# Optimization experiments

Measured on AMD Instinct MI355X. Metric: run time of the kernel, lower is better.

## Reference

```python
import jax, jax.numpy as jnp
import numpy as np

N = 100000   # nodes
D = 64       # node_emb_dim
R = 8        # num relations
E = 1600000  # edges (avg degree 16)


def setup_inputs() -> dict:
    key = jax.random.key(0)
    k1, k2, k3, k4, k5 = jax.random.split(key, 5)
    x = jax.random.normal(k1, (N, D), dtype=jnp.float32)
    edge_index = jax.random.randint(k2, (2, E), 0, N, dtype=jnp.int64)
    edge_type = jax.random.randint(k3, (E,), 0, R, dtype=jnp.int64)
    W_rel = jax.random.normal(k4, (R, D, D), dtype=jnp.float32) / np.sqrt(D)
    W_root = jax.random.normal(k5, (D, D), dtype=jnp.float32) / np.sqrt(D)
    bias = jnp.zeros((D,), dtype=jnp.float32)
    return {"x": x, "edge_index": edge_index, "edge_type": edge_type,
            "W_rel": W_rel, "W_root": W_root, "bias": bias}


def reference(x, edge_index, edge_type, W_rel, W_root, bias):
    # PyG RGCNConv: per-relation linear transform of source nodes,
    # mean-aggregated per (target node, relation), plus root transform + bias.
    n_nodes, d = x.shape
    n_rel = W_rel.shape[0]
    src, dst = edge_index[0], edge_index[1]

    # Transform every node under every relation once: [N, R, D]
    h_all = jnp.einsum('nd,rde->nre', x, W_rel)
    # Gather per-edge message: [E, D]
    msg = h_all[src, edge_type]

    # Per-(dst, relation) in-degree counts for mean normalization
    cnt = jnp.zeros((n_nodes, n_rel), dtype=x.dtype).at[dst, edge_type].add(1.0)
    norm = 1.0 / jnp.maximum(cnt[dst, edge_type], 1.0)  # [E]

    # Scatter-add normalized messages to target nodes
    agg = jnp.zeros((n_nodes, d), dtype=x.dtype).at[dst].add(msg * norm[:, None])

    out = agg + x @ W_root + bias
    return (out, edge_index, edge_type)
```

## Files before the change

### kernel.cpp

```cpp
#include <hip/hip_runtime.h>

#define DD 64
#define RR 8
#define KA 576
#define NT 18
#define NPART 8
#define ECH 2048
#define TILE 32

typedef short bf16x8 __attribute__((ext_vector_type(8)));
typedef float f32x4  __attribute__((ext_vector_type(4)));

__device__ __forceinline__ float bf2f(unsigned short u) {
    union { unsigned u; float f; } c; c.u = ((unsigned)u) << 16; return c.f;
}
__device__ __forceinline__ unsigned short f2bf(float f) {
    union { float f; unsigned u; } c; c.f = f;
    unsigned u = c.u;
    u += 0x7FFF + ((u >> 16) & 1);
    return (unsigned short)(u >> 16);
}

__global__ void k_xcast(const float* __restrict__ x, unsigned short* __restrict__ xb,
                        int N)
{
    int i = blockIdx.x * 256 + threadIdx.x;
    int total = (N + 1) * (DD / 4);
    if (i >= total) return;
    ushort4 o;
    if (i < N * (DD / 4)) {
        float4 f = ((const float4*)x)[i];
        o = make_ushort4(f2bf(f.x), f2bf(f.y), f2bf(f.z), f2bf(f.w));
    } else {
        o = make_ushort4(0, 0, 0, 0);
    }
    ((ushort4*)xb)[i] = o;
}

__global__ __launch_bounds__(256) void k_count_rank(
    const int* __restrict__ ei, const int* __restrict__ et,
    int* __restrict__ cnt, unsigned* __restrict__ rr, int E)
{
    const int base = blockIdx.x * ECH + threadIdx.x;
    int d[8], t[8], rk[8]; bool m[8];
    #pragma unroll
    for (int j = 0; j < 8; ++j) {
        int e = base + j * 256;
        m[j] = (e < E);
        d[j] = m[j] ? ei[E + e] : 0;
    }
    #pragma unroll
    for (int j = 0; j < 8; ++j) {
        int e = base + j * 256;
        if (m[j]) t[j] = et[e];
    }
    #pragma unroll
    for (int j = 0; j < 8; ++j)
        if (m[j]) rk[j] = atomicAdd(&cnt[(size_t)d[j] * RR + t[j]], 1);
    #pragma unroll
    for (int j = 0; j < 8; ++j) {
        int e = base + j * 256;
        if (m[j]) rr[e] = (unsigned)rk[j] | ((unsigned)t[j] << 24);
    }
}

__global__ __launch_bounds__(256) void k_alloc(
    const int* __restrict__ cnt, int* __restrict__ startv,
    int* __restrict__ start2, int* __restrict__ counter,
    int* __restrict__ sorted, int N)
{
    __shared__ int sdata[256];
    __shared__ int sbase;
    const int tid = threadIdx.x;
    const int n = blockIdx.x * 256 + tid;

    int deg = 0, deg8 = 0;
    int c[RR];
    if (n < N) {
        const int4* c4 = (const int4*)(cnt + (size_t)n * RR);
        int4 a = c4[0], b = c4[1];
        c[0]=a.x; c[1]=a.y; c[2]=a.z; c[3]=a.w;
        c[4]=b.x; c[5]=b.y; c[6]=b.z; c[7]=b.w;
        #pragma unroll
        for (int r = 0; r < RR; ++r) deg += c[r];
        deg8 = (deg + 7) & ~7;
    }
    sdata[tid] = deg8;
    __syncthreads();
    int v = deg8;
    #pragma unroll
    for (int off = 1; off < 256; off <<= 1) {
        int t = (tid >= off) ? sdata[tid - off] : 0;
        __syncthreads();
        v += t;
        sdata[tid] = v;
        __syncthreads();
    }
    if (tid == 255) sbase = atomicAdd(counter, v);
    __syncthreads();
    if (n < N) {
        int st = sbase + v - deg8;
        startv[n] = st;
        int h = st;
        #pragma unroll
        for (int r = 0; r < RR; ++r) { start2[(size_t)n * RR + r] = h; h += c[r]; }
        for (int j = deg; j < deg8; ++j) sorted[st + j] = N;
    }
}

__global__ __launch_bounds__(256) void k_scatter_part(
    const int* __restrict__ ei, const unsigned* __restrict__ rr,
    const int* __restrict__ start2, int* __restrict__ sorted, int E, int N)
{
    const int p    = blockIdx.x & (NPART - 1);
    const int sb   = blockIdx.x / NPART;
    const int dlo  = (int)((long long)N * p / NPART);
    const int dhi  = (int)((long long)N * (p + 1) / NPART);
    const int base = sb * ECH + threadIdx.x;

    int d[8]; bool m[8]; unsigned q[8]; int s[8], st[8];
    #pragma unroll
    for (int j = 0; j < 8; ++j) {
        int e = base + j * 256;
        d[j] = (e < E) ? ei[E + e] : -1;
    }
    #pragma unroll
    for (int j = 0; j < 8; ++j) m[j] = (d[j] >= dlo && d[j] < dhi);
    #pragma unroll
    for (int j = 0; j < 8; ++j) {
        int e = base + j * 256;
        if (m[j]) { q[j] = rr[e]; s[j] = ei[e]; }
    }
    #pragma unroll
    for (int j = 0; j < 8; ++j)
        if (m[j]) st[j] = start2[(size_t)d[j] * RR + (q[j] >> 24)];
    #pragma unroll
    for (int j = 0; j < 8; ++j)
        if (m[j]) sorted[st[j] + (q[j] & 0xFFFFFFu)] = s[j];
}

__global__ void k_packW(const float* __restrict__ Wrel, const float* __restrict__ Wroot,
                        unsigned short* __restrict__ Bh)
{
    int idx = blockIdx.x * 256 + threadIdx.x;
    if (idx >= NT * 4 * 64 * 8) return;
    int i    = idx & 7;
    int lane = (idx >> 3) & 63;
    int f    = (idx >> 9) & 3;
    int t    = idx >> 11;
    int k = t * 32 + (lane >> 4) * 8 + i;
    int d = f * 16 + (lane & 15);
    int r = k >> 6, kk = k & 63;
    float w = (r < RR) ? Wrel[((size_t)r * DD + kk) * DD + d]
                       : Wroot[(size_t)kk * DD + d];
    Bh[idx] = f2bf(w);
}

__global__ __launch_bounds__(512) void k_agg_mfma(
    const unsigned short* __restrict__ xb, const int* __restrict__ sorted,
    const int* __restrict__ startv, const int* __restrict__ cnt,
    const unsigned short* __restrict__ Bh, const float* __restrict__ bias,
    float* __restrict__ out, int N)
{
    __shared__ __align__(16) unsigned short As[TILE * KA];
    const int nb   = blockIdx.x * TILE;
    const int wv   = threadIdx.x >> 6;
    const int lane = threadIdx.x & 63;

    for (int i = 0; i < 4; ++i) {
        const int row = wv * 4 + i;
        const int dst = nb + row;
        if (dst >= N) break;

        const int xsh = (row & 7) << 3;
        unsigned short* ao = As + row * KA;

        const int cv = cnt[(size_t)dst * RR + (lane & 7)];
        int deg = 0;
        #pragma unroll
        for (int r = 0; r < RR; ++r) deg += __builtin_amdgcn_readlane(cv, r);
        const int deg8 = (deg + 7) & ~7;

        const int s0  = __builtin_amdgcn_readfirstlane(startv[dst]);
        const int end = s0 + deg8;

        int   r      = 0;
        int   c_r    = __builtin_amdgcn_readlane(cv, 0);
        int   next_b = s0 + c_r;
        float cur    = 0.f;

        auto flush = [&]() {
            float inv = __builtin_amdgcn_rcpf(fmaxf((float)c_r, 1.f));
            ao[(r * DD + lane) ^ xsh] = f2bf(cur * inv);
            cur = 0.f;
            ++r;
            c_r = __builtin_amdgcn_readlane(cv, r & 7);
            next_b += c_r;
        };

        int e = s0;
        int wbase = s0;
        int vidx  = sorted[wbase + lane];
        while (e < end) {
            if (e - wbase >= 64) {
                wbase = e;
                vidx  = sorted[wbase + lane];
            }
            const int k    = e - wbase;
            const int take = min(end - e, 64 - k);
            for (int ii = 0; ii < take; ii += 8) {
                int q0 = __builtin_amdgcn_readlane(vidx, k + ii + 0);
                int q1 = __builtin_amdgcn_readlane(vidx, k + ii + 1);
                int q2 = __builtin_amdgcn_readlane(vidx, k + ii + 2);
                int q3 = __builtin_amdgcn_readlane(vidx, k + ii + 3);
                int q4 = __builtin_amdgcn_readlane(vidx, k + ii + 4);
                int q5 = __builtin_amdgcn_readlane(vidx, k + ii + 5);
                int q6 = __builtin_amdgcn_readlane(vidx, k + ii + 6);
                int q7 = __builtin_amdgcn_readlane(vidx, k + ii + 7);
                unsigned short u0 = xb[(size_t)q0 * DD + lane];
                unsigned short u1 = xb[(size_t)q1 * DD + lane];
                unsigned short u2 = xb[(size_t)q2 * DD + lane];
                unsigned short u3 = xb[(size_t)q3 * DD + lane];
                unsigned short u4 = xb[(size_t)q4 * DD + lane];
                unsigned short u5 = xb[(size_t)q5 * DD + lane];
                unsigned short u6 = xb[(size_t)q6 * DD + lane];
                unsigned short u7 = xb[(size_t)q7 * DD + lane];
                const int base = e + ii;
                while (base + 0 == next_b && r < RR) flush();
                cur += bf2f(u0);
                while (base + 1 == next_b && r < RR) flush();
                cur += bf2f(u1);
                while (base + 2 == next_b && r < RR) flush();
                cur += bf2f(u2);
                while (base + 3 == next_b && r < RR) flush();
                cur += bf2f(u3);
                while (base + 4 == next_b && r < RR) flush();
                cur += bf2f(u4);
                while (base + 5 == next_b && r < RR) flush();
                cur += bf2f(u5);
                while (base + 6 == next_b && r < RR) flush();
                cur += bf2f(u6);
                while (base + 7 == next_b && r < RR) flush();
                cur += bf2f(u7);
            }
            e += take;
        }
        while (r < RR) flush();

        ao[(8 * DD + lane) ^ xsh] = xb[(size_t)dst * DD + lane];
    }

    __syncthreads();

    const int rlo = lane & 15;
    const int kg  = lane >> 4;
    const int rg  = (wv & 1) * 16;
    const int cf  = wv >> 1;
    const int row = rg + rlo;
    const int xsh = (row & 7) << 3;

    f32x4 acc = {0.f,0.f,0.f,0.f};

    const unsigned short* arow = As + row * KA;
    #pragma unroll
    for (int t = 0; t < NT; ++t) {
        bf16x8 a = *(const bf16x8*)(arow + ((t * 32 + kg * 8) ^ xsh));
        bf16x8 b = *(const bf16x8*)(Bh + (size_t)t * 2048 + (size_t)cf * 512
                                       + lane * 8);
        acc = __builtin_amdgcn_mfma_f32_16x16x32_bf16(a, b, acc, 0, 0, 0);
    }

    const float bl = bias[rlo + cf * 16];
    const int orow = nb + rg + kg * 4;
    #pragma unroll
    for (int j = 0; j < 4; ++j) {
        int rr2 = orow + j;
        if (rr2 < N) out[(size_t)rr2 * DD + rlo + cf * 16] = acc[j] + bl;
    }
}

__global__ void k_echo(const int* __restrict__ ei, const int* __restrict__ et,
                       float* __restrict__ out_ei, float* __restrict__ out_et,
                       int E)
{
    int i = blockIdx.x * 256 + threadIdx.x;
    if (i < 2 * E) out_ei[i] = (float)ei[i];
    if (i < E)     out_et[i] = (float)et[i];
}

extern "C" void kernel_launch(void* const* d_in, const int* in_sizes, int n_in,
                              void* d_out, int out_size, void* d_ws, size_t ws_size,
                              hipStream_t stream)
{
    const float* x     = (const float*)d_in[0];
    const int*   ei    = (const int*)d_in[1];
    const int*   et    = (const int*)d_in[2];
    const float* Wrel  = (const float*)d_in[3];
    const float* Wroot = (const float*)d_in[4];
    const float* bias  = (const float*)d_in[5];

    const int N = in_sizes[0] / DD;
    const int E = in_sizes[2];
    const int M = N * RR;

    float* out    = (float*)d_out;
    float* out_ei = out + (size_t)N * DD;
    float* out_et = out_ei + (size_t)2 * E;

    auto align = [](size_t v) { return (v + 255) & ~(size_t)255; };

    size_t p = 0;
    int* cnt = (int*)((char*)d_ws + p);              p += align((size_t)M * 4);
    int* counter = (int*)((char*)d_ws + p);
    size_t zero_bytes = p + 256;                     p += 256;
    int* startv = (int*)((char*)d_ws + p);           p += align((size_t)N * 4);
    int* start2 = (int*)((char*)d_ws + p);           p += align((size_t)M * 4);
    unsigned* rr = (unsigned*)((char*)d_ws + p);     p += align((size_t)E * 4);
    int* sorted = (int*)((char*)d_ws + p);           p += align(((size_t)E + 7*(size_t)N + 128) * 4);
    unsigned short* xb = (unsigned short*)((char*)d_ws + p); p += align(((size_t)N + 1) * DD * 2);
    unsigned short* Bh = (unsigned short*)((char*)d_ws + p); p += align((size_t)NT*4*64*8*2);

    hipMemsetAsync(d_ws, 0, zero_bytes, stream);

    const int nsb = (E + ECH - 1) / ECH;

    k_xcast <<<dim3(((N + 1) * (DD/4) + 255) / 256), 256, 0, stream>>>(x, xb, N);
    k_packW <<<dim3((NT*4*64*8 + 255) / 256), 256, 0, stream>>>(Wrel, Wroot, Bh);
    k_count_rank <<<dim3(nsb), 256, 0, stream>>>(ei, et, cnt, rr, E);
    k_alloc <<<dim3((N + 255) / 256), 256, 0, stream>>>(cnt, startv, start2,
                                                        counter, sorted, N);
    k_scatter_part<<<dim3(nsb * NPART), 256, 0, stream>>>(ei, rr, start2, sorted, E, N);

    k_agg_mfma<<<dim3((N + TILE - 1) / TILE), 512, 0, stream>>>(
        xb, sorted, startv, cnt, Bh, bias, out, N);

    k_echo<<<dim3((2 * E + 255) / 256), 256, 0, stream>>>(ei, et, out_ei, out_et, E);
}
```

Measured before the change: 224.2 us.

## Fuse edge echo into count kernel and gather four nodes per wave in one stream

The separate echo kernel is removed. Its float conversion of edge_index and edge_type is folded into the count/rank kernel, which already loads dst and type, so only src needs an extra read. The aggregation now treats each wave's four consecutive destination nodes as one contiguous segment of 32 relation runs, relying on those nodes being laid out contiguously with their padding in sorted order. This removes a kernel launch and repeated index loads, and lets the gather pipeline cross node boundaries. The cost is more complex boundary and padding bookkeeping in the flush logic.

```diff
diff --git a/kernel.cpp b/kernel.cpp
--- a/kernel.cpp
+++ b/kernel.cpp
@@ -37,12 +37,13 @@
     ((ushort4*)xb)[i] = o;
 }
 
-__global__ __launch_bounds__(256) void k_count_rank(
+__global__ __launch_bounds__(256) void k_count_rank_echo(
     const int* __restrict__ ei, const int* __restrict__ et,
-    int* __restrict__ cnt, unsigned* __restrict__ rr, int E)
+    int* __restrict__ cnt, unsigned* __restrict__ rr,
+    float* __restrict__ out_ei, float* __restrict__ out_et, int E)
 {
     const int base = blockIdx.x * ECH + threadIdx.x;
-    int d[8], t[8], rk[8]; bool m[8];
+    int d[8], t[8], s[8], rk[8]; bool m[8];
     #pragma unroll
     for (int j = 0; j < 8; ++j) {
         int e = base + j * 256;
@@ -52,7 +53,7 @@
     #pragma unroll
     for (int j = 0; j < 8; ++j) {
         int e = base + j * 256;
-        if (m[j]) t[j] = et[e];
+        if (m[j]) { t[j] = et[e]; s[j] = ei[e]; }
     }
     #pragma unroll
     for (int j = 0; j < 8; ++j)
@@ -60,7 +61,12 @@
     #pragma unroll
     for (int j = 0; j < 8; ++j) {
         int e = base + j * 256;
-        if (m[j]) rr[e] = (unsigned)rk[j] | ((unsigned)t[j] << 24);
+        if (m[j]) {
+            rr[e] = (unsigned)rk[j] | ((unsigned)t[j] << 24);
+            out_ei[e]     = (float)s[j];
+            out_ei[E + e] = (float)d[j];
+            out_et[e]     = (float)t[j];
+        }
     }
 }
 
@@ -167,35 +173,45 @@
     const int wv   = threadIdx.x >> 6;
     const int lane = threadIdx.x & 63;
 
-    for (int i = 0; i < 4; ++i) {
-        const int row = wv * 4 + i;
-        const int dst = nb + row;
-        if (dst >= N) break;
-
-        const int xsh = (row & 7) << 3;
-        unsigned short* ao = As + row * KA;
-
-        const int cv = cnt[(size_t)dst * RR + (lane & 7)];
-        int deg = 0;
+    const int row0 = wv * 4;
+    const int dst0 = nb + row0;
+    const int nv   = min(4, N - dst0);
+    if (nv > 0) {
+        int cidx = lane & 31;
+        if (cidx >= nv * 8) cidx = nv * 8 - 1;
+        const int cv = cnt[(size_t)dst0 * RR + cidx];
+
+        int pads = 0, total = 0;
         #pragma unroll
-        for (int r = 0; r < RR; ++r) deg += __builtin_amdgcn_readlane(cv, r);
-        const int deg8 = (deg + 7) & ~7;
-
-        const int s0  = __builtin_amdgcn_readfirstlane(startv[dst]);
-        const int end = s0 + deg8;
-
-        int   r      = 0;
-        int   c_r    = __builtin_amdgcn_readlane(cv, 0);
-        int   next_b = s0 + c_r;
+        for (int i = 0; i < 4; ++i) {
+            if (i < nv) {
+                int deg = 0;
+                #pragma unroll
+                for (int r = 0; r < RR; ++r)
+                    deg += __builtin_amdgcn_readlane(cv, i * 8 + r);
+                int d8 = (deg + 7) & ~7;
+                pads  |= (d8 - deg) << (3 * i);
+                total += d8;
+            }
+        }
+        const int nrun = nv * 8;
+        const int s0   = __builtin_amdgcn_readfirstlane(startv[dst0]);
+        const int end  = s0 + total;
+
+        int   rl     = 0;
+        int   next_b = s0 + __builtin_amdgcn_readlane(cv, 0);
         float cur    = 0.f;
 
         auto flush = [&]() {
-            float inv = __builtin_amdgcn_rcpf(fmaxf((float)c_r, 1.f));
-            ao[(r * DD + lane) ^ xsh] = f2bf(cur * inv);
+            const int c = __builtin_amdgcn_readlane(cv, rl & 31);
+            const float inv = __builtin_amdgcn_rcpf(fmaxf((float)c, 1.f));
+            const int row = row0 + (rl >> 3);
+            As[row * KA + (((rl & 7) * DD + lane) ^ ((row & 7) << 3))]
+                = f2bf(cur * inv);
             cur = 0.f;
-            ++r;
-            c_r = __builtin_amdgcn_readlane(cv, r & 7);
-            next_b += c_r;
+            ++rl;
+            const int cn = __builtin_amdgcn_readlane(cv, rl & 31);
+            next_b += cn + (((rl & 7) == 7) ? ((pads >> (3 * (rl >> 3))) & 7) : 0);
         };
 
         int e = s0;
@@ -226,28 +242,35 @@
                 unsigned short u6 = xb[(size_t)q6 * DD + lane];
                 unsigned short u7 = xb[(size_t)q7 * DD + lane];
                 const int base = e + ii;
-                while (base + 0 == next_b && r < RR) flush();
+                while (base + 0 == next_b && rl < nrun) flush();
                 cur += bf2f(u0);
-                while (base + 1 == next_b && r < RR) flush();
+                while (base + 1 == next_b && rl < nrun) flush();
                 cur += bf2f(u1);
-                while (base + 2 == next_b && r < RR) flush();
+                while (base + 2 == next_b && rl < nrun) flush();
                 cur += bf2f(u2);
-                while (base + 3 == next_b && r < RR) flush();
+                while (base + 3 == next_b && rl < nrun) flush();
                 cur += bf2f(u3);
-                while (base + 4 == next_b && r < RR) flush();
+                while (base + 4 == next_b && rl < nrun) flush();
                 cur += bf2f(u4);
-                while (base + 5 == next_b && r < RR) flush();
+                while (base + 5 == next_b && rl < nrun) flush();
                 cur += bf2f(u5);
-                while (base + 6 == next_b && r < RR) flush();
+                while (base + 6 == next_b && rl < nrun) flush();
                 cur += bf2f(u6);
-                while (base + 7 == next_b && r < RR) flush();
+                while (base + 7 == next_b && rl < nrun) flush();
                 cur += bf2f(u7);
             }
             e += take;
         }
-        while (r < RR) flush();
-
-        ao[(8 * DD + lane) ^ xsh] = xb[(size_t)dst * DD + lane];
+        while (rl < nrun) flush();
+
+        #pragma unroll
+        for (int i = 0; i < 4; ++i) {
+            if (i < nv) {
+                const int row = row0 + i;
+                As[row * KA + ((8 * DD + lane) ^ ((row & 7) << 3))]
+                    = xb[(size_t)(dst0 + i) * DD + lane];
+            }
+        }
     }
 
     __syncthreads();
@@ -277,15 +300,6 @@
         int rr2 = orow + j;
         if (rr2 < N) out[(size_t)rr2 * DD + rlo + cf * 16] = acc[j] + bl;
     }
-}
-
-__global__ void k_echo(const int* __restrict__ ei, const int* __restrict__ et,
-                       float* __restrict__ out_ei, float* __restrict__ out_et,
-                       int E)
-{
-    int i = blockIdx.x * 256 + threadIdx.x;
-    if (i < 2 * E) out_ei[i] = (float)ei[i];
-    if (i < E)     out_et[i] = (float)et[i];
 }
 
 extern "C" void kernel_launch(void* const* d_in, const int* in_sizes, int n_in,
@@ -326,13 +340,12 @@
 
     k_xcast <<<dim3(((N + 1) * (DD/4) + 255) / 256), 256, 0, stream>>>(x, xb, N);
     k_packW <<<dim3((NT*4*64*8 + 255) / 256), 256, 0, stream>>>(Wrel, Wroot, Bh);
-    k_count_rank <<<dim3(nsb), 256, 0, stream>>>(ei, et, cnt, rr, E);
+    k_count_rank_echo <<<dim3(nsb), 256, 0, stream>>>(ei, et, cnt, rr,
+                                                      out_ei, out_et, E);
     k_alloc <<<dim3((N + 255) / 256), 256, 0, stream>>>(cnt, startv, start2,
                                                         counter, sorted, N);
     k_scatter_part<<<dim3(nsb * NPART), 256, 0, stream>>>(ei, rr, start2, sorted, E, N);
 
     k_agg_mfma<<<dim3((N + TILE - 1) / TILE), 512, 0, stream>>>(
         xb, sorted, startv, cnt, Bh, bias, out, N);
-
-    k_echo<<<dim3((2 * E + 255) / 256), 256, 0, stream>>>(ei, et, out_ei, out_et, E);
-}
+}
```

After: 234.3 us. 1.05x slower.

## Fuse edge echo into count kernel and batch per-wave count/start loads

Applied to the files above, without the earlier changes.

The separate echo kernel that converts edge_index and edge_type to float is removed. That conversion now happens inside the count/rank kernel, which already reads dst and type and now also reads src. This saves one launch and a second full read of the edge arrays. In the aggregation kernel, each wave now loads the counts and start offsets for its four rows with one vector load and extracts them with readlane, instead of issuing per-row loads. The trade-off is extra register pressure and more stores in the count kernel, which is atomic-bound.

```diff
diff --git a/kernel.cpp b/kernel.cpp
--- a/kernel.cpp
+++ b/kernel.cpp
@@ -37,12 +37,13 @@
     ((ushort4*)xb)[i] = o;
 }
 
-__global__ __launch_bounds__(256) void k_count_rank(
+__global__ __launch_bounds__(256) void k_count_rank_echo(
     const int* __restrict__ ei, const int* __restrict__ et,
-    int* __restrict__ cnt, unsigned* __restrict__ rr, int E)
+    int* __restrict__ cnt, unsigned* __restrict__ rr,
+    float* __restrict__ out_ei, float* __restrict__ out_et, int E)
 {
     const int base = blockIdx.x * ECH + threadIdx.x;
-    int d[8], t[8], rk[8]; bool m[8];
+    int d[8], t[8], s[8], rk[8]; bool m[8];
     #pragma unroll
     for (int j = 0; j < 8; ++j) {
         int e = base + j * 256;
@@ -52,7 +53,7 @@
     #pragma unroll
     for (int j = 0; j < 8; ++j) {
         int e = base + j * 256;
-        if (m[j]) t[j] = et[e];
+        if (m[j]) { t[j] = et[e]; s[j] = ei[e]; }
     }
     #pragma unroll
     for (int j = 0; j < 8; ++j)
@@ -60,7 +61,12 @@
     #pragma unroll
     for (int j = 0; j < 8; ++j) {
         int e = base + j * 256;
-        if (m[j]) rr[e] = (unsigned)rk[j] | ((unsigned)t[j] << 24);
+        if (m[j]) {
+            rr[e] = (unsigned)rk[j] | ((unsigned)t[j] << 24);
+            out_ei[e]     = (float)s[j];
+            out_ei[E + e] = (float)d[j];
+            out_et[e]     = (float)t[j];
+        }
     }
 }
 
@@ -167,87 +173,99 @@
     const int wv   = threadIdx.x >> 6;
     const int lane = threadIdx.x & 63;
 
-    for (int i = 0; i < 4; ++i) {
-        const int row = wv * 4 + i;
-        const int dst = nb + row;
-        if (dst >= N) break;
-
-        const int xsh = (row & 7) << 3;
-        unsigned short* ao = As + row * KA;
-
-        const int cv = cnt[(size_t)dst * RR + (lane & 7)];
-        int deg = 0;
-        #pragma unroll
-        for (int r = 0; r < RR; ++r) deg += __builtin_amdgcn_readlane(cv, r);
-        const int deg8 = (deg + 7) & ~7;
-
-        const int s0  = __builtin_amdgcn_readfirstlane(startv[dst]);
-        const int end = s0 + deg8;
-
-        int   r      = 0;
-        int   c_r    = __builtin_amdgcn_readlane(cv, 0);
-        int   next_b = s0 + c_r;
-        float cur    = 0.f;
-
-        auto flush = [&]() {
-            float inv = __builtin_amdgcn_rcpf(fmaxf((float)c_r, 1.f));
-            ao[(r * DD + lane) ^ xsh] = f2bf(cur * inv);
-            cur = 0.f;
-            ++r;
-            c_r = __builtin_amdgcn_readlane(cv, r & 7);
-            next_b += c_r;
-        };
-
-        int e = s0;
-        int wbase = s0;
-        int vidx  = sorted[wbase + lane];
-        while (e < end) {
-            if (e - wbase >= 64) {
-                wbase = e;
-                vidx  = sorted[wbase + lane];
+    const int row0 = wv * 4;
+    const int dst0 = nb + row0;
+    const int nv   = min(4, N - dst0);
+    if (nv > 0) {
+        int cidx = lane & 31;
+        if (cidx >= nv * 8) cidx = nv * 8 - 1;
+        const int cv = cnt[(size_t)dst0 * RR + cidx];
+        int sidx = lane & 3;
+        if (sidx >= nv) sidx = nv - 1;
+        const int sv = startv[dst0 + sidx];
+
+        for (int i = 0; i < 4; ++i) {
+            if (i >= nv) break;
+            const int row = row0 + i;
+            const int dst = dst0 + i;
+            const int xsh = (row & 7) << 3;
+            unsigned short* ao = As + row * KA;
+            const int cb = i * 8;
+
+            int deg = 0;
+            #pragma unroll
+            for (int r = 0; r < RR; ++r)
+                deg += __builtin_amdgcn_readlane(cv, cb + r);
+            const int deg8 = (deg + 7) & ~7;
+
+            const int s0  = __builtin_amdgcn_readlane(sv, i);
+            const int end = s0 + deg8;
+
+            int   r      = 0;
+            int   c_r    = __builtin_amdgcn_readlane(cv, cb);
+            int   next_b = s0 + c_r;
+            float cur    = 0.f;
+
+            auto flush = [&]() {
+                float inv = __builtin_amdgcn_rcpf(fmaxf((float)c_r, 1.f));
+                ao[(r * DD + lane) ^ xsh] = f2bf(cur * inv);
+                cur = 0.f;
+                ++r;
+                c_r = __builtin_amdgcn_readlane(cv, cb + (r & 7));
+                next_b += c_r;
+            };
+
+            int e = s0;
+            int wbase = s0;
+            int vidx  = sorted[wbase + lane];
+            while (e < end) {
+                if (e - wbase >= 64) {
+                    wbase = e;
+                    vidx  = sorted[wbase + lane];
+                }
+                const int k    = e - wbase;
+                const int take = min(end - e, 64 - k);
+                for (int ii = 0; ii < take; ii += 8) {
+                    int q0 = __builtin_amdgcn_readlane(vidx, k + ii + 0);
+                    int q1 = __builtin_amdgcn_readlane(vidx, k + ii + 1);
+                    int q2 = __builtin_amdgcn_readlane(vidx, k + ii + 2);
+                    int q3 = __builtin_amdgcn_readlane(vidx, k + ii + 3);
+                    int q4 = __builtin_amdgcn_readlane(vidx, k + ii + 4);
+                    int q5 = __builtin_amdgcn_readlane(vidx, k + ii + 5);
+                    int q6 = __builtin_amdgcn_readlane(vidx, k + ii + 6);
+                    int q7 = __builtin_amdgcn_readlane(vidx, k + ii + 7);
+                    unsigned short u0 = xb[(size_t)q0 * DD + lane];
+                    unsigned short u1 = xb[(size_t)q1 * DD + lane];
+                    unsigned short u2 = xb[(size_t)q2 * DD + lane];
+                    unsigned short u3 = xb[(size_t)q3 * DD + lane];
+                    unsigned short u4 = xb[(size_t)q4 * DD + lane];
+                    unsigned short u5 = xb[(size_t)q5 * DD + lane];
+                    unsigned short u6 = xb[(size_t)q6 * DD + lane];
+                    unsigned short u7 = xb[(size_t)q7 * DD + lane];
+                    const int base = e + ii;
+                    while (base + 0 == next_b && r < RR) flush();
+                    cur += bf2f(u0);
+                    while (base + 1 == next_b && r < RR) flush();
+                    cur += bf2f(u1);
+                    while (base + 2 == next_b && r < RR) flush();
+                    cur += bf2f(u2);
+                    while (base + 3 == next_b && r < RR) flush();
+                    cur += bf2f(u3);
+                    while (base + 4 == next_b && r < RR) flush();
+                    cur += bf2f(u4);
+                    while (base + 5 == next_b && r < RR) flush();
+                    cur += bf2f(u5);
+                    while (base + 6 == next_b && r < RR) flush();
+                    cur += bf2f(u6);
+                    while (base + 7 == next_b && r < RR) flush();
+                    cur += bf2f(u7);
+                }
+                e += take;
             }
-            const int k    = e - wbase;
-            const int take = min(end - e, 64 - k);
-            for (int ii = 0; ii < take; ii += 8) {
-                int q0 = __builtin_amdgcn_readlane(vidx, k + ii + 0);
-                int q1 = __builtin_amdgcn_readlane(vidx, k + ii + 1);
-                int q2 = __builtin_amdgcn_readlane(vidx, k + ii + 2);
-                int q3 = __builtin_amdgcn_readlane(vidx, k + ii + 3);
-                int q4 = __builtin_amdgcn_readlane(vidx, k + ii + 4);
-                int q5 = __builtin_amdgcn_readlane(vidx, k + ii + 5);
-                int q6 = __builtin_amdgcn_readlane(vidx, k + ii + 6);
-                int q7 = __builtin_amdgcn_readlane(vidx, k + ii + 7);
-                unsigned short u0 = xb[(size_t)q0 * DD + lane];
-                unsigned short u1 = xb[(size_t)q1 * DD + lane];
-                unsigned short u2 = xb[(size_t)q2 * DD + lane];
-                unsigned short u3 = xb[(size_t)q3 * DD + lane];
-                unsigned short u4 = xb[(size_t)q4 * DD + lane];
-                unsigned short u5 = xb[(size_t)q5 * DD + lane];
-                unsigned short u6 = xb[(size_t)q6 * DD + lane];
-                unsigned short u7 = xb[(size_t)q7 * DD + lane];
-                const int base = e + ii;
-                while (base + 0 == next_b && r < RR) flush();
-                cur += bf2f(u0);
-                while (base + 1 == next_b && r < RR) flush();
-                cur += bf2f(u1);
-                while (base + 2 == next_b && r < RR) flush();
-                cur += bf2f(u2);
-                while (base + 3 == next_b && r < RR) flush();
-                cur += bf2f(u3);
-                while (base + 4 == next_b && r < RR) flush();
-                cur += bf2f(u4);
-                while (base + 5 == next_b && r < RR) flush();
-                cur += bf2f(u5);
-                while (base + 6 == next_b && r < RR) flush();
-                cur += bf2f(u6);
-                while (base + 7 == next_b && r < RR) flush();
-                cur += bf2f(u7);
-            }
-            e += take;
+            while (r < RR) flush();
+
+            ao[(8 * DD + lane) ^ xsh] = xb[(size_t)dst * DD + lane];
         }
-        while (r < RR) flush();
-
-        ao[(8 * DD + lane) ^ xsh] = xb[(size_t)dst * DD + lane];
     }
 
     __syncthreads();
@@ -277,15 +295,6 @@
         int rr2 = orow + j;
         if (rr2 < N) out[(size_t)rr2 * DD + rlo + cf * 16] = acc[j] + bl;
     }
-}
-
-__global__ void k_echo(const int* __restrict__ ei, const int* __restrict__ et,
-                       float* __restrict__ out_ei, float* __restrict__ out_et,
-                       int E)
-{
-    int i = blockIdx.x * 256 + threadIdx.x;
-    if (i < 2 * E) out_ei[i] = (float)ei[i];
-    if (i < E)     out_et[i] = (float)et[i];
 }
 
 extern "C" void kernel_launch(void* const* d_in, const int* in_sizes, int n_in,
@@ -326,13 +335,12 @@
 
     k_xcast <<<dim3(((N + 1) * (DD/4) + 255) / 256), 256, 0, stream>>>(x, xb, N);
     k_packW <<<dim3((NT*4*64*8 + 255) / 256), 256, 0, stream>>>(Wrel, Wroot, Bh);
-    k_count_rank <<<dim3(nsb), 256, 0, stream>>>(ei, et, cnt, rr, E);
+    k_count_rank_echo <<<dim3(nsb), 256, 0, stream>>>(ei, et, cnt, rr,
+                                                      out_ei, out_et, E);
     k_alloc <<<dim3((N + 255) / 256), 256, 0, stream>>>(cnt, startv, start2,
                                                         counter, sorted, N);
     k_scatter_part<<<dim3(nsb * NPART), 256, 0, stream>>>(ei, rr, start2, sorted, E, N);
 
     k_agg_mfma<<<dim3((N + TILE - 1) / TILE), 512, 0, stream>>>(
         xb, sorted, startv, cnt, Bh, bias, out, N);
-
-    k_echo<<<dim3((2 * E + 255) / 256), 256, 0, stream>>>(ei, et, out_ei, out_et, E);
-}
+}
```

Measured after the change: 218.6 us. -2.5%, faster.
